# Kernel tuning notes

Hardware: AMD Instinct MI355X
Metric: run time of the kernel (lower is better)

## Reference

```python
import jax, jax.numpy as jnp
import numpy as np

ITERATIONS = 5


def _dilate3x3(x):
    # 3x3 box 'conv' with all-ones kernel, padding=1 (SAME), single channel, NCHW
    k = jnp.ones((1, 1, 3, 3), x.dtype)
    return jax.lax.conv_general_dilated(
        x, k, window_strides=(1, 1), padding='SAME',
        dimension_numbers=('NCHW', 'OIHW', 'NCHW'))


def setup_inputs() -> dict:
    key = jax.random.key(0)
    k1, k2 = jax.random.split(key)
    H = W = 4096
    prediction = jax.random.uniform(k1, (1, 1, H, W), dtype=jnp.float32)
    ground_truth = jax.random.uniform(k2, (1, 1, H, W), dtype=jnp.float32)
    return {"prediction": prediction, "ground_truth": ground_truth}


def reference(prediction, ground_truth):
    # distance_weight = [1, 4, 9, 16, 25]
    weights = jnp.asarray([(i + 1) ** 2 for i in range(ITERATIONS)], dtype=jnp.float32)
    gt_sum = jnp.sum(ground_truth)
    fn_total = jnp.zeros((), dtype=jnp.float32)
    pred = prediction
    for i in range(ITERATIONS):  # fixed small unrolled loop (sequential recurrence)
        dilated = jnp.clip(_dilate3x3(pred), 0.0, 1.0)
        sharp = jax.nn.sigmoid(20.0 * (dilated - pred - 0.5))
        false_negative = ground_truth * sharp
        fn_total = fn_total + weights[i] * jnp.sum(false_negative) / gt_sum
        pred = pred + false_negative  # fed into next iteration's dilation
    return fn_total
```

## Files before the change

### kernel.cpp

```cpp
#include <hip/hip_runtime.h>

#define N 4096
#define CORE_W 116
#define NSTRIP 36
#define ROWS 18
#define NCHUNK 228
#define ITERS 5
#define NSLOT 32
#define WPB 4


typedef float2 f2;
__device__ __forceinline__ f2 mkf2(float a, float b){ f2 r; r.x=a; r.y=b; return r; }

__device__ __forceinline__ f2 hsum(f2 v) {
    float m = v.x + v.y;
    float L = __shfl_up(v.y, 1);
    float R = __shfl_down(v.x, 1);
    return mkf2(L + m, m + R);
}

__device__ __forceinline__ f2 stepf(f2 p, f2 d, f2 g, f2* fn) {
    const float C1 = 28.853900817779268f;
    const float C2 = 14.426950408889634f;
    f2 o, f;
    {
        float dd = fminf(fmaxf(d.x, 0.f), 1.f);
        float u  = __builtin_fmaf(p.x - dd, C1, C2);
        float sh = __builtin_amdgcn_rcpf(1.f + __builtin_amdgcn_exp2f(u));
        f.x = g.x * sh; o.x = p.x + f.x;
    }
    {
        float dd = fminf(fmaxf(d.y, 0.f), 1.f);
        float u  = __builtin_fmaf(p.y - dd, C1, C2);
        float sh = __builtin_amdgcn_rcpf(1.f + __builtin_amdgcn_exp2f(u));
        f.y = g.y * sh; o.y = p.y + f.y;
    }
    *fn = f;
    return o;
}

__device__ __forceinline__ f2 ldrow(const float* __restrict__ base, int row,
                                    int gc, bool edge) {
    if (row < 0 || row >= N) return mkf2(0.f, 0.f);
    if (!edge) return *(const f2*)(base + (size_t)row * N + gc);
    float a = 0.f, b = 0.f;
    if (gc >= 0 && gc < N)         a = base[(size_t)row * N + gc];
    if (gc + 1 >= 0 && gc + 1 < N) b = base[(size_t)row * N + gc + 1];
    return mkf2(a, b);
}

__global__ __launch_bounds__(64 * WPB) void wlc_main(
    const float* __restrict__ pred,
    const float* __restrict__ gt,
    float* __restrict__ ws)
{
    const int tid  = threadIdx.x;
    const int lane = tid & 63;
    const int wid  = blockIdx.x * WPB + (tid >> 6);
    const int strip = wid % NSTRIP;
    const int chunk = wid / NSTRIP;

    const int x0 = strip * CORE_W - 6;
    const int gc = x0 + 2 * lane;
    const bool edge = (strip == 0) || (strip == NSTRIP - 1);

    const int R0 = chunk * ROWS;
    const int R1 = min(R0 + ROWS, N);
    const int t0 = R0 - 5;
    const int t1 = R1 + 5;

    const float colm = (lane >= 3 && lane <= 60) ? 1.f : 0.f;
    const float m0 = (gc     < N) ? colm : 0.f;
    const float m1 = (gc + 1 < N) ? colm : 0.f;

    f2 pr[6], gb[6];
    f2 h0[3], h1[3], h2[3], h3[3], h4[3];
    f2 o1[2], o2[2], o3[2], o4[2];
#pragma unroll
    for (int i = 0; i < 6; ++i) { pr[i] = mkf2(0,0); gb[i] = mkf2(0,0); }
#pragma unroll
    for (int i = 0; i < 3; ++i) { h0[i]=h1[i]=h2[i]=h3[i]=h4[i]=mkf2(0,0); }
#pragma unroll
    for (int i = 0; i < 2; ++i) { o1[i]=o2[i]=o3[i]=o4[i]=mkf2(0,0); }

    pr[2] = ldrow(pred, t0,     gc, edge);
    pr[3] = ldrow(pred, t0 + 1, gc, edge);

    float s1a=0.f, s2a=0.f, s3a=0.f, s4a=0.f, s5a=0.f, gsa=0.f;

#define S6(o) ((8 + k + (o)) % 6)
#define S3(o) ((8 + k + (o)) % 3)
#define S2(o) ((8 + k + (o)) % 2)

    for (int tb = t0; tb < t1; tb += 6) {
#pragma unroll
        for (int k = 0; k < 6; ++k) {
            const int t = tb + k;
            if (t < t1) {
                const f2 g5 = gb[S6(-5)];
                if (t + 2 <= R1 + 4) pr[S6(2)] = ldrow(pred, t + 2, gc, edge);
                if (t + 1 <= R1 + 3) gb[S6(1)] = ldrow(gt,   t + 1, gc, edge);

                h0[S3(0)] = hsum(pr[S6(0)]);

                f2 d, fn, o;
                d = mkf2(h0[0].x + h0[1].x + h0[2].x, h0[0].y + h0[1].y + h0[2].y);
                o = stepf(pr[S6(-1)], d, gb[S6(-1)], &fn);
                { int r = t - 1; if (r >= R0 && r < R1) s1a += fn.x*m0 + fn.y*m1; }
                h1[S3(-1)] = hsum(o);  o1[S2(-1)] = o;

                d = mkf2(h1[0].x + h1[1].x + h1[2].x, h1[0].y + h1[1].y + h1[2].y);
                o = stepf(o1[S2(-2)], d, gb[S6(-2)], &fn);
                { int r = t - 2; if (r >= R0 && r < R1) s2a += fn.x*m0 + fn.y*m1; }
                h2[S3(-2)] = hsum(o);  o2[S2(-2)] = o;

                d = mkf2(h2[0].x + h2[1].x + h2[2].x, h2[0].y + h2[1].y + h2[2].y);
                o = stepf(o2[S2(-3)], d, gb[S6(-3)], &fn);
                { int r = t - 3; if (r >= R0 && r < R1) s3a += fn.x*m0 + fn.y*m1; }
                h3[S3(-3)] = hsum(o);  o3[S2(-3)] = o;

                d = mkf2(h3[0].x + h3[1].x + h3[2].x, h3[0].y + h3[1].y + h3[2].y);
                o = stepf(o3[S2(-4)], d, gb[S6(-4)], &fn);
                { int r = t - 4; if (r >= R0 && r < R1) s4a += fn.x*m0 + fn.y*m1; }
                h4[S3(-4)] = hsum(o);  o4[S2(-4)] = o;

                d = mkf2(h4[0].x + h4[1].x + h4[2].x, h4[0].y + h4[1].y + h4[2].y);
                o = stepf(o4[S2(-5)], d, g5, &fn);
                { int r = t - 5;
                  if (r >= R0 && r < R1) {
                      s5a += fn.x*m0 + fn.y*m1;
                      gsa += g5.x*m0 + g5.y*m1;
                  } }
            }
        }
    }
#undef S6
#undef S3
#undef S2

    float vals[6] = {gsa, s1a, s2a, s3a, s4a, s5a};
    const int slot = wid & (NSLOT - 1);
#pragma unroll
    for (int kk = 0; kk < 6; ++kk) {
        float v = vals[kk];
#pragma unroll
        for (int off = 32; off > 0; off >>= 1)
            v += __shfl_down(v, off, 64);
        if (lane == 0) atomicAdd(&ws[slot * 32 + kk], v);
    }
}

__global__ void wlc_final(const float* __restrict__ ws, float* __restrict__ out)
{
    float t[6] = {0.f, 0.f, 0.f, 0.f, 0.f, 0.f};
    for (int s = 0; s < NSLOT; ++s)
#pragma unroll
        for (int kk = 0; kk < 6; ++kk)
            t[kk] += ws[s * 32 + kk];
    out[0] = (1.f * t[1] + 4.f * t[2] + 9.f * t[3] + 16.f * t[4] + 25.f * t[5]) / t[0];
}

extern "C" void kernel_launch(void* const* d_in, const int* in_sizes, int n_in,
                              void* d_out, int out_size, void* d_ws, size_t ws_size,
                              hipStream_t stream)
{
    const float* pred = (const float*)d_in[0];
    const float* gtp  = (const float*)d_in[1];
    float* ws = (float*)d_ws;

    hipMemsetAsync(d_ws, 0, NSLOT * 32 * sizeof(float), stream);

    wlc_main<<<dim3((NSTRIP * NCHUNK) / WPB), 64 * WPB, 0, stream>>>(pred, gtp, ws);
    wlc_final<<<1, 1, 0, stream>>>(ws, (float*)d_out);
}
```

Before: 229.7 us.

## Skew iteration stages by two rows to break serial dependency chain

Reorders the five fused dilation stages so that each stage works on a row two steps behind the previous one, processed in reverse order. Within one row step the stages become independent, which exposes instruction-level parallelism instead of a serial chain of shuffles and transcendentals. Row chunk height grows from 18 to 30 to amortize the larger halo (7 leading, 10 trailing rows). The ground-truth ring buffer and the unroll both double, which raises register pressure and may lower occupancy.

```diff
diff --git a/kernel.cpp b/kernel.cpp
--- a/kernel.cpp
+++ b/kernel.cpp
@@ -3,9 +3,8 @@
 #define N 4096
 #define CORE_W 116
 #define NSTRIP 36
-#define ROWS 18
-#define NCHUNK 228
-#define ITERS 5
+#define ROWS 30
+#define NCHUNK 137
 #define NSLOT 32
 #define WPB 4
 
@@ -18,6 +17,10 @@
     float L = __shfl_up(v.y, 1);
     float R = __shfl_down(v.x, 1);
     return mkf2(L + m, m + R);
+}
+
+__device__ __forceinline__ f2 add3(f2 a, f2 b, f2 c) {
+    return mkf2(a.x + b.x + c.x, a.y + b.y + c.y);
 }
 
 __device__ __forceinline__ f2 stepf(f2 p, f2 d, f2 g, f2* fn) {
@@ -67,75 +70,90 @@
 
     const int R0 = chunk * ROWS;
     const int R1 = min(R0 + ROWS, N);
-    const int t0 = R0 - 5;
-    const int t1 = R1 + 5;
+    const int t0 = R0 - 7;
+    const int t1 = R1 + 10;
 
     const float colm = (lane >= 3 && lane <= 60) ? 1.f : 0.f;
     const float m0 = (gc     < N) ? colm : 0.f;
     const float m1 = (gc + 1 < N) ? colm : 0.f;
 
-    f2 pr[6], gb[6];
+    f2 pr[6], gb[12];
     f2 h0[3], h1[3], h2[3], h3[3], h4[3];
     f2 o1[2], o2[2], o3[2], o4[2];
 #pragma unroll
-    for (int i = 0; i < 6; ++i) { pr[i] = mkf2(0,0); gb[i] = mkf2(0,0); }
+    for (int i = 0; i < 6; ++i)  pr[i] = mkf2(0,0);
+#pragma unroll
+    for (int i = 0; i < 12; ++i) gb[i] = mkf2(0,0);
 #pragma unroll
     for (int i = 0; i < 3; ++i) { h0[i]=h1[i]=h2[i]=h3[i]=h4[i]=mkf2(0,0); }
 #pragma unroll
     for (int i = 0; i < 2; ++i) { o1[i]=o2[i]=o3[i]=o4[i]=mkf2(0,0); }
 
-    pr[2] = ldrow(pred, t0,     gc, edge);
-    pr[3] = ldrow(pred, t0 + 1, gc, edge);
+    pr[0] = ldrow(pred, t0,     gc, edge);
+    pr[1] = ldrow(pred, t0 + 1, gc, edge);
+    pr[2] = ldrow(pred, t0 + 2, gc, edge);
 
     float s1a=0.f, s2a=0.f, s3a=0.f, s4a=0.f, s5a=0.f, gsa=0.f;
 
-#define S6(o) ((8 + k + (o)) % 6)
-#define S3(o) ((8 + k + (o)) % 3)
-#define S2(o) ((8 + k + (o)) % 2)
+#define S6(o)  ((k + (o) + 6)  % 6)
+#define S12(o) ((k + (o) + 12) % 12)
+#define S3(o)  ((k + (o) + 12) % 3)
+#define S2(o)  ((k + (o) + 10) % 2)
 
-    for (int tb = t0; tb < t1; tb += 6) {
+    for (int tb = t0; tb < t1; tb += 12) {
 #pragma unroll
-        for (int k = 0; k < 6; ++k) {
+        for (int k = 0; k < 12; ++k) {
             const int t = tb + k;
             if (t < t1) {
-                const f2 g5 = gb[S6(-5)];
-                if (t + 2 <= R1 + 4) pr[S6(2)] = ldrow(pred, t + 2, gc, edge);
-                if (t + 1 <= R1 + 3) gb[S6(1)] = ldrow(gt,   t + 1, gc, edge);
-
-                h0[S3(0)] = hsum(pr[S6(0)]);
+                if (t + 3 <= R1 + 4) pr[S6(3)]  = ldrow(pred, t + 3, gc, edge);
+                if (t + 1 <= R1 + 3) gb[S12(1)] = ldrow(gt,   t + 1, gc, edge);
 
                 f2 d, fn, o;
-                d = mkf2(h0[0].x + h0[1].x + h0[2].x, h0[0].y + h0[1].y + h0[2].y);
-                o = stepf(pr[S6(-1)], d, gb[S6(-1)], &fn);
-                { int r = t - 1; if (r >= R0 && r < R1) s1a += fn.x*m0 + fn.y*m1; }
-                h1[S3(-1)] = hsum(o);  o1[S2(-1)] = o;
 
-                d = mkf2(h1[0].x + h1[1].x + h1[2].x, h1[0].y + h1[1].y + h1[2].y);
-                o = stepf(o1[S2(-2)], d, gb[S6(-2)], &fn);
-                { int r = t - 2; if (r >= R0 && r < R1) s2a += fn.x*m0 + fn.y*m1; }
-                h2[S3(-2)] = hsum(o);  o2[S2(-2)] = o;
-
-                d = mkf2(h2[0].x + h2[1].x + h2[2].x, h2[0].y + h2[1].y + h2[2].y);
-                o = stepf(o2[S2(-3)], d, gb[S6(-3)], &fn);
-                { int r = t - 3; if (r >= R0 && r < R1) s3a += fn.x*m0 + fn.y*m1; }
-                h3[S3(-3)] = hsum(o);  o3[S2(-3)] = o;
-
-                d = mkf2(h3[0].x + h3[1].x + h3[2].x, h3[0].y + h3[1].y + h3[2].y);
-                o = stepf(o3[S2(-4)], d, gb[S6(-4)], &fn);
-                { int r = t - 4; if (r >= R0 && r < R1) s4a += fn.x*m0 + fn.y*m1; }
-                h4[S3(-4)] = hsum(o);  o4[S2(-4)] = o;
-
-                d = mkf2(h4[0].x + h4[1].x + h4[2].x, h4[0].y + h4[1].y + h4[2].y);
-                o = stepf(o4[S2(-5)], d, g5, &fn);
-                { int r = t - 5;
-                  if (r >= R0 && r < R1) {
-                      s5a += fn.x*m0 + fn.y*m1;
-                      gsa += g5.x*m0 + g5.y*m1;
-                  } }
+                {
+                    const f2 g5 = gb[S12(-10)];
+                    d = add3(h4[S3(-11)], h4[S3(-10)], h4[S3(-9)]);
+                    o = stepf(o4[S2(-10)], d, g5, &fn);
+                    int r = t - 10;
+                    if (r >= R0 && r < R1) {
+                        s5a += fn.x*m0 + fn.y*m1;
+                        gsa += g5.x*m0 + g5.y*m1;
+                    }
+                }
+                {
+                    d = add3(h3[S3(-9)], h3[S3(-8)], h3[S3(-7)]);
+                    o = stepf(o3[S2(-8)], d, gb[S12(-8)], &fn);
+                    int r = t - 8;
+                    if (r >= R0 && r < R1) s4a += fn.x*m0 + fn.y*m1;
+                    h4[S3(-8)] = hsum(o);  o4[S2(-8)] = o;
+                }
+                {
+                    d = add3(h2[S3(-7)], h2[S3(-6)], h2[S3(-5)]);
+                    o = stepf(o2[S2(-6)], d, gb[S12(-6)], &fn);
+                    int r = t - 6;
+                    if (r >= R0 && r < R1) s3a += fn.x*m0 + fn.y*m1;
+                    h3[S3(-6)] = hsum(o);  o3[S2(-6)] = o;
+                }
+                {
+                    d = add3(h1[S3(-5)], h1[S3(-4)], h1[S3(-3)]);
+                    o = stepf(o1[S2(-4)], d, gb[S12(-4)], &fn);
+                    int r = t - 4;
+                    if (r >= R0 && r < R1) s2a += fn.x*m0 + fn.y*m1;
+                    h2[S3(-4)] = hsum(o);  o2[S2(-4)] = o;
+                }
+                {
+                    d = add3(h0[S3(-3)], h0[S3(-2)], h0[S3(-1)]);
+                    o = stepf(pr[S6(-2)], d, gb[S12(-2)], &fn);
+                    int r = t - 2;
+                    if (r >= R0 && r < R1) s1a += fn.x*m0 + fn.y*m1;
+                    h1[S3(-2)] = hsum(o);  o1[S2(-2)] = o;
+                }
+                h0[S3(0)] = hsum(pr[S6(0)]);
             }
         }
     }
 #undef S6
+#undef S12
 #undef S3
 #undef S2
 
```

Result: slower. 234.7 us (+2.1%).
